# Kernel optimization log

Measured on AMD Instinct MI355X. Metric: run time of the kernel, lower is better.

The kernel has to match this reference:

```python
import jax, jax.numpy as jnp
import numpy as np

S, B, F = 2048, 2, 100          # seq, batch(datasets), n_features
E, NHEAD, NHID, L = 512, 8, 1024, 4  # emsize, heads, ffn hidden, encoder layers
H, NOUT, DEC = 128, 10, 2048    # predicted hidden size, n_out, decoder embed dim
SEP = 1024                      # single_eval_pos
TOTAL = H + F * H + H + H * H + NOUT + H * NOUT  # 30730 flat predicted params


def setup_inputs():
    key = jax.random.key(0)
    ks = jax.random.split(key, 12)
    w = lambda k, sh: jax.random.normal(k, sh, jnp.float32) * 0.02
    z = lambda sh: jnp.zeros(sh, jnp.float32)
    o = lambda sh: jnp.ones(sh, jnp.float32)
    return {
        'x': jax.random.normal(ks[0], (S, B, F), jnp.float32),
        'y': jax.random.normal(ks[1], (S, B), jnp.float32),
        'enc_w': w(ks[2], (E, F)), 'enc_b': z((E,)),
        'yenc_w': w(ks[3], (E, 1)), 'yenc_b': z((E,)),
        'qkv_w': w(ks[4], (L, 3 * E, E)), 'qkv_b': z((L, 3 * E)),
        'out_w': w(ks[5], (L, E, E)), 'out_b': z((L, E)),
        'ln1_g': o((L, E)), 'ln1_b': z((L, E)),
        'ln2_g': o((L, E)), 'ln2_b': z((L, E)),
        'ff1_w': w(ks[6], (L, NHID, E)), 'ff1_b': z((L, NHID)),
        'ff2_w': w(ks[7], (L, E, NHID)), 'ff2_b': z((L, E)),
        'dec_w1': w(ks[8], (DEC, E)), 'dec_b1': z((DEC,)),
        'dec_w2': w(ks[9], (TOTAL, DEC)), 'dec_b2': z((TOTAL,)),
        'single_eval_pos': SEP,
    }


def _ln(x, g, b):
    m = x.mean(-1, keepdims=True)
    v = x.var(-1, keepdims=True)
    return (x - m) / jnp.sqrt(v + 1e-5) * g + b


def _mha(x, wqkv, bqkv, wo, bo):
    s, b, e = x.shape
    hd = e // NHEAD
    qkv = x @ wqkv.T + bqkv                        # [s,b,3e]
    q, k, v = jnp.split(qkv, 3, axis=-1)
    q = q.reshape(s, b, NHEAD, hd)
    k = k.reshape(s, b, NHEAD, hd)
    v = v.reshape(s, b, NHEAD, hd)
    att = jnp.einsum('sbhd,tbhd->bhst', q, k) / np.float32(np.sqrt(hd))
    p = jax.nn.softmax(att, axis=-1)
    o = jnp.einsum('bhst,tbhd->sbhd', p, v).reshape(s, b, e)
    return o @ wo.T + bo


def _forward(x, y, enc_w, enc_b, yenc_w, yenc_b, qkv_w, qkv_b, out_w, out_b,
             ln1_g, ln1_b, ln2_g, ln2_b, ff1_w, ff1_b, ff2_w, ff2_b,
             dec_w1, dec_b1, dec_w2, dec_b2, sep):
    b_sz = x.shape[1]
    # encoders (Linear with replace_nan_by_zero=True)
    x_enc = jnp.nan_to_num(x) @ enc_w.T + enc_b                # [S,B,E]
    y_enc = y[..., None] @ yenc_w.T + yenc_b                   # [S,B,E]
    h = x_enc[:sep] + y_enc[:sep]                              # [sep,B,E]
    # transformer encoder backbone (post-norm, gelu)
    for i in range(L):
        a = _mha(h, qkv_w[i], qkv_b[i], out_w[i], out_b[i])
        h = _ln(h + a, ln1_g[i], ln1_b[i])
        f = jax.nn.gelu(h @ ff1_w[i].T + ff1_b[i]) @ ff2_w[i].T + ff2_b[i]
        h = _ln(h + f, ln2_g[i], ln2_b[i])
    # decoder: mean-pool over train tokens -> MLP -> flat predicted weights
    pooled = h.mean(0)                                         # [B,E]
    d = jax.nn.relu(pooled @ dec_w1.T + dec_b1)
    flat = d @ dec_w2.T + dec_b2                               # [B,TOTAL]
    off = 0
    b1 = flat[:, off:off + H]; off += H
    w1 = flat[:, off:off + F * H].reshape(b_sz, F, H); off += F * H
    b2 = flat[:, off:off + H]; off += H
    w2 = flat[:, off:off + H * H].reshape(b_sz, H, H); off += H * H
    b3 = flat[:, off:off + NOUT]; off += NOUT
    w3 = flat[:, off:off + H * NOUT].reshape(b_sz, H, NOUT)
    # apply predicted per-dataset MLP to test points
    xt = jnp.nan_to_num(x[sep:])                               # [S-sep,B,F]
    t = jnp.einsum('sbf,bfh->sbh', xt, w1) + b1                # (x[...,None]*w1).sum(2)+b1
    t = jnp.einsum('sbh,bhk->sbk', jax.nn.relu(t), w2) + b2
    t = jnp.einsum('sbh,bhk->sbk', jax.nn.relu(t), w3) + b3
    return t                                                   # [S-sep,B,NOUT]


def reference(x, y, enc_w, enc_b, yenc_w, yenc_b, qkv_w, qkv_b, out_w, out_b,
              ln1_g, ln1_b, ln2_g, ln2_b, ff1_w, ff1_b, ff2_w, ff2_b,
              dec_w1, dec_b1, dec_w2, dec_b2, single_eval_pos):
    return _forward(x, y, enc_w, enc_b, yenc_w, yenc_b, qkv_w, qkv_b, out_w, out_b,
                    ln1_g, ln1_b, ln2_g, ln2_b, ff1_w, ff1_b, ff2_w, ff2_b,
                    dec_w1, dec_b1, dec_w2, dec_b2, single_eval_pos)
```

## Files before the change

kernel.cpp:

```cpp
#include <hip/hip_runtime.h>


#define BATCH  2
#define FDIM   100
#define EDIM   512
#define NHEADS 8
#define HD     64
#define NHID   1024
#define NLAYER 4
#define HDIM   128
#define NOUTD  10
#define DECD   2048
#define SEPP   1024
#define TOTALW 30730
#define NTOK   2048

typedef unsigned short u16;
typedef __attribute__((ext_vector_type(8))) short bf16x8;
typedef __attribute__((ext_vector_type(4))) float f32x4;

__device__ __forceinline__ float nanfix(float v) {
    if (isnan(v)) return 0.f;
    if (isinf(v)) return v > 0.f ? 3.4028234663852886e38f : -3.4028234663852886e38f;
    return v;
}
__device__ __forceinline__ u16 f2bf(float f) {
    unsigned u = __float_as_uint(f);
    u += 0x7fffu + ((u >> 16) & 1u);
    return (u16)(u >> 16);
}
__device__ __forceinline__ float bf2f(u16 h) {
    return __uint_as_float(((unsigned)h) << 16);
}
__device__ __forceinline__ bf16x8 scale8(bf16x8 a, float s) {
    bf16x8 r;
    #pragma unroll
    for (int i = 0; i < 8; i++) {
        float v = bf2f((u16)a[i]) * s;
        r[i] = (short)f2bf(v);
    }
    return r;
}

#define GLOAD16(gsrc, ldst) \
    __builtin_amdgcn_global_load_lds( \
        (const __attribute__((address_space(1))) void*)(gsrc), \
        (__attribute__((address_space(3))) void*)(ldst), 16, 0, 0)

__global__ __launch_bounds__(256) void gemm2(
    const u16* __restrict__ A, int lda,
    const u16* __restrict__ B, int ldb,
    void* __restrict__ Cv, int ldc, int cbf,
    int K, long long zCstride, float alpha,
    const float* __restrict__ bias, int act,
    u16* __restrict__ vtout)
{
    __shared__ __align__(16) u16 lds[3][8192];

    int tid = threadIdx.x;
    int lane = tid & 63, w = tid >> 6;
    int wr = w >> 1, wc = w & 1;
    int mBase = blockIdx.y * 64, nBase = blockIdx.x * 64;
    int r16 = lane & 15, kg = lane >> 4;
    long long zk = (long long)blockIdx.z * K;
    long long offC = (long long)blockIdx.z * zCstride;

    int c0 = w * 64 + lane;
    int c1 = 256 + w * 64 + lane;
    int r0 = c0 >> 3, r1 = c1 >> 3;
    int e0 = ((((c0 & 7) * 16) ^ ((r0 & 7) << 4)) >> 1);
    int e1 = ((((c1 & 7) * 16) ^ ((r1 & 7) << 4)) >> 1);
    const u16* sA0 = A + (long long)(mBase + r0) * lda + e0 + zk;
    const u16* sA1 = A + (long long)(mBase + r1) * lda + e1 + zk;
    const u16* sB0 = B + (long long)(nBase + r0) * ldb + e0 + zk;
    const u16* sB1 = B + (long long)(nBase + r1) * ldb + e1 + zk;
    int dA0 = w * 512, dA1 = 2048 + w * 512;
    int dB0 = 4096 + w * 512, dB1 = 6144 + w * 512;

    int ra0 = wr * 32 + r16,      ra1 = wr * 32 + 16 + r16;
    int rb0 = wc * 32 + r16,      rb1 = wc * 32 + 16 + r16;
    int cb0 = kg * 16;
    int cb1 = 64 + kg * 16;
    int oa00 = (ra0 * 128 + (cb0 ^ ((ra0 & 7) << 4))) >> 1;
    int oa01 = (ra0 * 128 + (cb1 ^ ((ra0 & 7) << 4))) >> 1;
    int oa10 = (ra1 * 128 + (cb0 ^ ((ra1 & 7) << 4))) >> 1;
    int oa11 = (ra1 * 128 + (cb1 ^ ((ra1 & 7) << 4))) >> 1;
    int ob00 = 4096 + ((rb0 * 128 + (cb0 ^ ((rb0 & 7) << 4))) >> 1);
    int ob01 = 4096 + ((rb0 * 128 + (cb1 ^ ((rb0 & 7) << 4))) >> 1);
    int ob10 = 4096 + ((rb1 * 128 + (cb0 ^ ((rb1 & 7) << 4))) >> 1);
    int ob11 = 4096 + ((rb1 * 128 + (cb1 ^ ((rb1 & 7) << 4))) >> 1);

    f32x4 acc00 = {0.f, 0.f, 0.f, 0.f};
    f32x4 acc01 = acc00, acc10 = acc00, acc11 = acc00;

    int nt = K >> 6;

#define STAGE2(t, bi) { int ko_ = (t) << 6; \
    GLOAD16(sA0 + ko_, &lds[bi][dA0]); \
    GLOAD16(sA1 + ko_, &lds[bi][dA1]); \
    GLOAD16(sB0 + ko_, &lds[bi][dB0]); \
    GLOAD16(sB1 + ko_, &lds[bi][dB1]); }

    STAGE2(0, 0);
    STAGE2(1, 1);

    int cur = 0;
    for (int t = 0; t < nt; t++) {
        if (t == nt - 1) {
            asm volatile("s_waitcnt vmcnt(0)" ::: "memory");
        } else {
            asm volatile("s_waitcnt vmcnt(4)" ::: "memory");
        }
        __builtin_amdgcn_s_barrier();
        if (t + 2 < nt) {
            int tgt = cur - 1; if (tgt < 0) tgt += 3;
            STAGE2(t + 2, tgt);
        }
        const u16* L = &lds[cur][0];
        bf16x8 a0 = *(const bf16x8*)(L + oa00);
        bf16x8 a1 = *(const bf16x8*)(L + oa10);
        bf16x8 b0 = *(const bf16x8*)(L + ob00);
        bf16x8 b1 = *(const bf16x8*)(L + ob10);
        acc00 = __builtin_amdgcn_mfma_f32_16x16x32_bf16(a0, b0, acc00, 0, 0, 0);
        acc01 = __builtin_amdgcn_mfma_f32_16x16x32_bf16(a0, b1, acc01, 0, 0, 0);
        acc10 = __builtin_amdgcn_mfma_f32_16x16x32_bf16(a1, b0, acc10, 0, 0, 0);
        acc11 = __builtin_amdgcn_mfma_f32_16x16x32_bf16(a1, b1, acc11, 0, 0, 0);
        a0 = *(const bf16x8*)(L + oa01);
        a1 = *(const bf16x8*)(L + oa11);
        b0 = *(const bf16x8*)(L + ob01);
        b1 = *(const bf16x8*)(L + ob11);
        acc00 = __builtin_amdgcn_mfma_f32_16x16x32_bf16(a0, b0, acc00, 0, 0, 0);
        acc01 = __builtin_amdgcn_mfma_f32_16x16x32_bf16(a0, b1, acc01, 0, 0, 0);
        acc10 = __builtin_amdgcn_mfma_f32_16x16x32_bf16(a1, b0, acc10, 0, 0, 0);
        acc11 = __builtin_amdgcn_mfma_f32_16x16x32_bf16(a1, b1, acc11, 0, 0, 0);
        cur++; if (cur == 3) cur = 0;
    }
#undef STAGE2

    if (vtout && nBase >= 1024) {
        u16* T = &lds[0][0];
        __syncthreads();
        #pragma unroll
        for (int i = 0; i < 2; i++) {
            #pragma unroll
            for (int j = 0; j < 2; j++) {
                f32x4 v = (i == 0) ? (j == 0 ? acc00 : acc01) : (j == 0 ? acc10 : acc11);
                int dl = wc * 32 + j * 16 + r16;
                float bv = bias ? bias[nBase + dl] : 0.f;
                #pragma unroll
                for (int r = 0; r < 4; r++) {
                    int ml = wr * 32 + i * 16 + kg * 4 + r;
                    T[ml * 64 + dl] = f2bf(v[r] * alpha + bv);
                }
            }
        }
        __syncthreads();
        int d = tid & 63, cbv = (tid >> 6) & 1, half = tid >> 7;
        int hh = (nBase - 1024) >> 6;
        long long orow = ((long long)(cbv * 8 + hh) * 64 + d) * 1024 + (mBase >> 1) + half * 16;
        bf16x8 v0, v1;
        #pragma unroll
        for (int k = 0; k < 8; k++) {
            v0[k] = (short)T[((half * 16 + k) * 2 + cbv) * 64 + d];
            v1[k] = (short)T[((half * 16 + 8 + k) * 2 + cbv) * 64 + d];
        }
        *(bf16x8*)(vtout + orow) = v0;
        *(bf16x8*)(vtout + orow + 8) = v1;
        return;
    }

    #pragma unroll
    for (int i = 0; i < 2; i++) {
        #pragma unroll
        for (int j = 0; j < 2; j++) {
            f32x4 v = (i == 0) ? (j == 0 ? acc00 : acc01) : (j == 0 ? acc10 : acc11);
            int col = nBase + wc * 32 + j * 16 + r16;
            float bv = bias ? bias[col] : 0.f;
            long long base = offC + (long long)(mBase + wr * 32 + i * 16 + kg * 4) * ldc + col;
            #pragma unroll
            for (int r = 0; r < 4; r++) {
                float c = v[r] * alpha + bv;
                if (act == 2) {
                    float u = 0.7978845608028654f * (c + 0.044715f * c * c * c);
                    c = 0.5f * c * (1.f + tanhf(u));
                }
                if (cbf) ((u16*)Cv)[base + (long long)r * ldc] = f2bf(c);
                else     ((float*)Cv)[base + (long long)r * ldc] = c;
            }
        }
    }
}

__global__ __launch_bounds__(1024) void flash_attn(
    const u16* __restrict__ qkvb, const u16* __restrict__ vtm,
    u16* __restrict__ attnb)
{
    int qt = blockIdx.x;
    int bh = blockIdx.y;
    int cb = bh >> 3, hh = bh & 7;
    int tid = threadIdx.x;
    int w = tid >> 6, lane = tid & 63;
    int p = w & 3, qf = w >> 2;
    int r16 = lane & 15, kg = lane >> 4;

    __shared__ __align__(16) u16 plds[16][2048];
    u16* pl = &plds[w][0];

    int qrow = qt * 64 + p * 16 + r16;
    const u16* qp = qkvb + ((long long)qrow * 2 + cb) * 1536 + hh * 64 + kg * 8;
    bf16x8 qf0 = scale8(*(const bf16x8*)(qp), 0.125f);
    bf16x8 qf1 = scale8(*(const bf16x8*)(qp + 32), 0.125f);

    const u16* kbase = qkvb + (long long)cb * 1536 + 512 + hh * 64;
    const u16* vbase = vtm + ((long long)bh * 64) * 1024;

    f32x4 l = {0.f, 0.f, 0.f, 0.f};
    f32x4 o[4] = {};

    int rb0 = (((r16 * 64 + kg * 8) * 2) ^ ((r16 & 7) << 4)) >> 1;
    int rb1 = (((r16 * 64 + 32 + kg * 8) * 2) ^ ((r16 & 7) << 4)) >> 1;

    for (int kt = qf * 4; kt < qf * 4 + 4; kt++) {
        f32x4 s[4];
        #pragma unroll
        for (int nb = 0; nb < 4; nb++) {
            int key = kt * 64 + nb * 16 + r16;
            const u16* kp = kbase + (long long)key * 3072 + kg * 8;
            bf16x8 kf0 = *(const bf16x8*)(kp);
            bf16x8 kf1 = *(const bf16x8*)(kp + 32);
            f32x4 acc = {};
            acc = __builtin_amdgcn_mfma_f32_16x16x32_bf16(qf0, kf0, acc, 0, 0, 0);
            acc = __builtin_amdgcn_mfma_f32_16x16x32_bf16(qf1, kf1, acc, 0, 0, 0);
            s[nb] = acc;
        }
        f32x4 rs = {};
        #pragma unroll
        for (int nb = 0; nb < 4; nb++)
            #pragma unroll
            for (int r = 0; r < 4; r++) {
                float pv = __expf(s[nb][r]);
                s[nb][r] = pv;
                rs[r] += pv;
            }
        #pragma unroll
        for (int off = 1; off < 16; off <<= 1) {
            #pragma unroll
            for (int r = 0; r < 4; r++) rs[r] += __shfl_xor(rs[r], off);
        }
        #pragma unroll
        for (int r = 0; r < 4; r++) l[r] += rs[r];

        #pragma unroll
        for (int nb = 0; nb < 4; nb++)
            #pragma unroll
            for (int r = 0; r < 4; r++) {
                int row = kg * 4 + r;
                int col = nb * 16 + r16;
                int byi = (((row * 64 + col) * 2) ^ ((row & 7) << 4)) >> 1;
                pl[byi] = f2bf(s[nb][r]);
            }

        bf16x8 pa0 = *(const bf16x8*)(pl + rb0);
        bf16x8 pa1 = *(const bf16x8*)(pl + rb1);
        #pragma unroll
        for (int db = 0; db < 4; db++) {
            const u16* vp = vbase + (long long)(db * 16 + r16) * 1024 + kt * 64 + kg * 8;
            bf16x8 vf0 = *(const bf16x8*)(vp);
            bf16x8 vf1 = *(const bf16x8*)(vp + 32);
            o[db] = __builtin_amdgcn_mfma_f32_16x16x32_bf16(pa0, vf0, o[db], 0, 0, 0);
            o[db] = __builtin_amdgcn_mfma_f32_16x16x32_bf16(pa1, vf1, o[db], 0, 0, 0);
        }
    }

    __syncthreads();
    float* fb = (float*)&plds[0][0];
    if (qf < 3) {
        int base = ((qf * 4 + p) * 64 + lane) * 20;
        #pragma unroll
        for (int r = 0; r < 4; r++) fb[base + r] = l[r];
        #pragma unroll
        for (int db = 0; db < 4; db++)
            #pragma unroll
            for (int r = 0; r < 4; r++) fb[base + 4 + db * 4 + r] = o[db][r];
    }
    __syncthreads();
    if (qf == 3) {
        #pragma unroll
        for (int q2 = 0; q2 < 3; q2++) {
            int base = ((q2 * 4 + p) * 64 + lane) * 20;
            #pragma unroll
            for (int r = 0; r < 4; r++) l[r] += fb[base + r];
            #pragma unroll
            for (int db = 0; db < 4; db++)
                #pragma unroll
                for (int r = 0; r < 4; r++) o[db][r] += fb[base + 4 + db * 4 + r];
        }
        f32x4 linv;
        #pragma unroll
        for (int r = 0; r < 4; r++) linv[r] = 1.f / l[r];
        #pragma unroll
        for (int db = 0; db < 4; db++)
            #pragma unroll
            for (int r = 0; r < 4; r++) {
                float val = o[db][r] * linv[r];
                int row = qt * 64 + p * 16 + kg * 4 + r;
                attnb[((long long)row * 2 + cb) * 512 + hh * 64 + db * 16 + r16] = f2bf(val);
            }
    }
}

__global__ __launch_bounds__(256) void cvt_all(
    const float* __restrict__ s0, const float* __restrict__ s1,
    const float* __restrict__ s2, const float* __restrict__ s3,
    u16* __restrict__ d0, u16* __restrict__ d1,
    u16* __restrict__ d2, u16* __restrict__ d3)
{
    const int n0 = 3145728, n1 = 1048576, n2 = 2097152, n3 = 2097152;
    int i = blockIdx.x * 256 + threadIdx.x;
    int st = gridDim.x * 256;
    for (; i < n0 + n1 + n2 + n3; i += st) {
        if (i < n0) d0[i] = f2bf(s0[i]);
        else if (i < n0 + n1) d1[i - n0] = f2bf(s1[i - n0]);
        else if (i < n0 + n1 + n2) d2[i - n0 - n1] = f2bf(s2[i - n0 - n1]);
        else d3[i - n0 - n1 - n2] = f2bf(s3[i - n0 - n1 - n2]);
    }
}

__global__ __launch_bounds__(512) void encoder_kernel(
    const float* __restrict__ x, const float* __restrict__ y,
    const float* __restrict__ enc_w, const float* __restrict__ enc_b,
    const float* __restrict__ yenc_w, const float* __restrict__ yenc_b,
    float* __restrict__ h, u16* __restrict__ h_bf)
{
    int g = blockIdx.x;
    int tid = threadIdx.x;
    __shared__ float xs[16][FDIM];
    __shared__ float ys[16];
    for (int i = tid; i < 16 * FDIM; i += 512) {
        int tk = i / FDIM, f = i % FDIM;
        xs[tk][f] = nanfix(x[(long long)(g * 16 + tk) * FDIM + f]);
    }
    if (tid < 16) ys[tid] = y[g * 16 + tid];
    __syncthreads();
    float base = enc_b[tid] + yenc_b[tid];
    float yw = yenc_w[tid];
    const float* wr = enc_w + (long long)tid * FDIM;
    float acc[16];
    #pragma unroll
    for (int j = 0; j < 16; j++) acc[j] = 0.f;
    for (int f = 0; f < FDIM; f++) {
        float wv = wr[f];
        #pragma unroll
        for (int j = 0; j < 16; j++) acc[j] = fmaf(xs[j][f], wv, acc[j]);
    }
    #pragma unroll
    for (int j = 0; j < 16; j++) {
        float v = base + ys[j] * yw + acc[j];
        long long t = g * 16 + j;
        h[t * EDIM + tid] = v;
        h_bf[t * EDIM + tid] = f2bf(v);
    }
}

__global__ __launch_bounds__(256) void add_ln3_kernel(
    const float* a, const float* __restrict__ p0, const float* __restrict__ p1,
    const float* __restrict__ cbias,
    const float* __restrict__ g, const float* __restrict__ be,
    float* out, u16* __restrict__ out_bf)
{
    int row = blockIdx.x;
    int tid = threadIdx.x;
    const float* pa = a + (long long)row * EDIM;
    const float* pr0 = p0 + (long long)row * EDIM;
    const float* pr1 = p1 + (long long)row * EDIM;
    float v0 = pa[tid] + pr0[tid] + pr1[tid] + cbias[tid];
    float v1 = pa[tid + 256] + pr0[tid + 256] + pr1[tid + 256] + cbias[tid + 256];
    float s = v0 + v1, q = v0 * v0 + v1 * v1;
    #pragma unroll
    for (int off = 32; off; off >>= 1) {
        s += __shfl_xor(s, off);
        q += __shfl_xor(q, off);
    }
    __shared__ float ss[4], sq[4];
    int w = tid >> 6, lane = tid & 63;
    if (lane == 0) { ss[w] = s; sq[w] = q; }
    __syncthreads();
    s = ss[0] + ss[1] + ss[2] + ss[3];
    q = sq[0] + sq[1] + sq[2] + sq[3];
    float mean = s * (1.f / EDIM);
    float var = q * (1.f / EDIM) - mean * mean;
    float rstd = rsqrtf(var + 1e-5f);
    float o0 = (v0 - mean) * rstd * g[tid] + be[tid];
    float o1 = (v1 - mean) * rstd * g[tid + 256] + be[tid + 256];
    float* po = out + (long long)row * EDIM;
    u16* pb = out_bf + (long long)row * EDIM;
    po[tid] = o0;        po[tid + 256] = o1;
    pb[tid] = f2bf(o0);  pb[tid + 256] = f2bf(o1);
}

__global__ __launch_bounds__(1024) void pool1_kernel(
    const float* __restrict__ h, float* __restrict__ part)
{
    int j = blockIdx.x;
    int idx = threadIdx.x;
    float s = 0.f;
    #pragma unroll 8
    for (int k = 0; k < 32; k++)
        s += h[(long long)(j * 32 + k) * 1024 + idx];
    part[j * 1024 + idx] = s;
}
__global__ __launch_bounds__(1024) void pool2_kernel(
    const float* __restrict__ part, float* __restrict__ pooled)
{
    int idx = threadIdx.x;
    float s = 0.f;
    #pragma unroll 8
    for (int j = 0; j < 32; j++) s += part[j * 1024 + idx];
    pooled[idx] = s * (1.f / 1024.f);
}

__global__ __launch_bounds__(256) void wavedot2_kernel(
    const float* __restrict__ v0, const float* __restrict__ v1,
    const float* __restrict__ W, const float* __restrict__ bias,
    float* __restrict__ out0, float* __restrict__ out1,
    int R, int K, int act)
{
    int gw = (blockIdx.x * 256 + threadIdx.x) >> 6;
    int lane = threadIdx.x & 63;
    int nw = (gridDim.x * 256) >> 6;
    const float4* x0 = (const float4*)v0;
    const float4* x1 = (const float4*)v1;
    for (int r = gw; r < R; r += nw) {
        const float4* w4 = (const float4*)(W + (long long)r * K);
        float a0 = 0.f, a1 = 0.f;
        for (int i = lane; i < (K >> 2); i += 64) {
            float4 w = w4[i];
            float4 p = x0[i];
            float4 q = x1[i];
            a0 += w.x * p.x + w.y * p.y + w.z * p.z + w.w * p.w;
            a1 += w.x * q.x + w.y * q.y + w.z * q.z + w.w * q.w;
        }
        #pragma unroll
        for (int off = 32; off; off >>= 1) {
            a0 += __shfl_xor(a0, off);
            a1 += __shfl_xor(a1, off);
        }
        if (lane == 0) {
            float bb = bias[r];
            float o0 = a0 + bb, o1 = a1 + bb;
            if (act == 1) { o0 = fmaxf(o0, 0.f); o1 = fmaxf(o1, 0.f); }
            out0[r] = o0; out1[r] = o1;
        }
    }
}

__global__ __launch_bounds__(128) void final_mlp_kernel(
    const float* __restrict__ x, const float* __restrict__ flat,
    float* __restrict__ out)
{
    int g = blockIdx.x;
    int b = g >> 7;
    int j0 = (g & 127) * 8;
    int tid = threadIdx.x;
    const float* fl = flat + (long long)b * TOTALW;
    __shared__ float xs[8][FDIM], t1s[8][HDIM], t2s[8][HDIM];
    for (int i = tid; i < 8 * FDIM; i += 128) {
        int j = i / FDIM, f = i % FDIM;
        int t = (j0 + j) * 2 + b;
        xs[j][f] = nanfix(x[(long long)(NTOK + t) * FDIM + f]);
    }
    __syncthreads();
    {
        float acc[8];
        float b1 = fl[tid];
        #pragma unroll
        for (int j = 0; j < 8; j++) acc[j] = b1;
        const float* w1 = fl + HDIM;
        for (int f = 0; f < FDIM; f++) {
            float wv = w1[f * HDIM + tid];
            #pragma unroll
            for (int j = 0; j < 8; j++) acc[j] = fmaf(xs[j][f], wv, acc[j]);
        }
        #pragma unroll
        for (int j = 0; j < 8; j++) t1s[j][tid] = fmaxf(acc[j], 0.f);
    }
    __syncthreads();
    {
        float acc[8];
        float b2 = fl[12928 + tid];
        #pragma unroll
        for (int j = 0; j < 8; j++) acc[j] = b2;
        const float* w2 = fl + 13056;
        for (int hh = 0; hh < HDIM; hh++) {
            float wv = w2[hh * HDIM + tid];
            #pragma unroll
            for (int j = 0; j < 8; j++) acc[j] = fmaf(t1s[j][hh], wv, acc[j]);
        }
        #pragma unroll
        for (int j = 0; j < 8; j++) t2s[j][tid] = fmaxf(acc[j], 0.f);
    }
    __syncthreads();
    if (tid < NOUTD) {
        float acc[8];
        float b3 = fl[29440 + tid];
        #pragma unroll
        for (int j = 0; j < 8; j++) acc[j] = b3;
        const float* w3 = fl + 29450;
        for (int hh = 0; hh < HDIM; hh++) {
            float wv = w3[hh * NOUTD + tid];
            #pragma unroll
            for (int j = 0; j < 8; j++) acc[j] = fmaf(t2s[j][hh], wv, acc[j]);
        }
        #pragma unroll
        for (int j = 0; j < 8; j++) {
            int t = (j0 + j) * 2 + b;
            out[(long long)t * NOUTD + tid] = acc[j];
        }
    }
}

extern "C" void kernel_launch(void* const* d_in, const int* in_sizes, int n_in,
                              void* d_out, int out_size, void* d_ws, size_t ws_size,
                              hipStream_t stream) {
    const float* x      = (const float*)d_in[0];
    const float* y      = (const float*)d_in[1];
    const float* enc_w  = (const float*)d_in[2];
    const float* enc_b  = (const float*)d_in[3];
    const float* yenc_w = (const float*)d_in[4];
    const float* yenc_b = (const float*)d_in[5];
    const float* qkv_w  = (const float*)d_in[6];
    const float* qkv_b  = (const float*)d_in[7];
    const float* out_w  = (const float*)d_in[8];
    const float* out_b  = (const float*)d_in[9];
    const float* ln1_g  = (const float*)d_in[10];
    const float* ln1_b  = (const float*)d_in[11];
    const float* ln2_g  = (const float*)d_in[12];
    const float* ln2_b  = (const float*)d_in[13];
    const float* ff1_w  = (const float*)d_in[14];
    const float* ff1_b  = (const float*)d_in[15];
    const float* ff2_w  = (const float*)d_in[16];
    const float* ff2_b  = (const float*)d_in[17];
    const float* dec_w1 = (const float*)d_in[18];
    const float* dec_b1 = (const float*)d_in[19];
    const float* dec_w2 = (const float*)d_in[20];
    const float* dec_b2 = (const float*)d_in[21];

    float* ws     = (float*)d_ws;
    float* h      = ws;
    u16*   h_bf   = (u16*)(h + 1048576);
    u16*   qkv_bf = h_bf + 1048576;
    u16*   vt     = qkv_bf + 3145728;
    u16*   attn_bf= vt + 1048576;
    u16*   ffb_bf = attn_bf + 1048576;
    u16*   wq     = ffb_bf + 2097152;
    u16*   wo     = wq + 3145728;
    u16*   wf1    = wo + 1048576;
    u16*   wf2    = wf1 + 2097152;
    float* big    = (float*)(wf2 + 2097152);
    float* big2   = big + 1048576;
    float* part   = big2 + 1048576;
    float* pooled = part + 32768;
    float* dbuf   = pooled + 1024;
    float* flat   = dbuf + 4096;

    cvt_all<<<4096, 256, 0, stream>>>(qkv_w, out_w, ff1_w, ff2_w, wq, wo, wf1, wf2);

    encoder_kernel<<<128, 512, 0, stream>>>(x, y, enc_w, enc_b, yenc_w, yenc_b, h, h_bf);

    const long long PSTRIDE = (long long)NTOK * EDIM;

    for (int l = 0; l < NLAYER; l++) {
        gemm2<<<dim3(24, 32, 1), 256, 0, stream>>>(
            h_bf, EDIM, wq + (size_t)l * 786432, EDIM,
            qkv_bf, 1536, 1, EDIM, 0, 1.f, qkv_b + (size_t)l * 1536, 0, vt);

        flash_attn<<<dim3(16, 16), 1024, 0, stream>>>(qkv_bf, vt, attn_bf);

        gemm2<<<dim3(8, 32, 2), 256, 0, stream>>>(
            attn_bf, EDIM, wo + (size_t)l * 262144, EDIM,
            big, EDIM, 0, 256, PSTRIDE, 1.f, nullptr, 0, nullptr);

        add_ln3_kernel<<<NTOK, 256, 0, stream>>>(h, big, big2,
            out_b + (size_t)l * EDIM,
            ln1_g + (size_t)l * EDIM, ln1_b + (size_t)l * EDIM, h, h_bf);

        gemm2<<<dim3(16, 32, 1), 256, 0, stream>>>(
            h_bf, EDIM, wf1 + (size_t)l * 524288, EDIM,
            ffb_bf, NHID, 1, EDIM, 0, 1.f, ff1_b + (size_t)l * NHID, 2, nullptr);

        gemm2<<<dim3(8, 32, 2), 256, 0, stream>>>(
            ffb_bf, NHID, wf2 + (size_t)l * 524288, NHID,
            big, EDIM, 0, 512, PSTRIDE, 1.f, nullptr, 0, nullptr);

        add_ln3_kernel<<<NTOK, 256, 0, stream>>>(h, big, big2,
            ff2_b + (size_t)l * EDIM,
            ln2_g + (size_t)l * EDIM, ln2_b + (size_t)l * EDIM, h, h_bf);
    }

    pool1_kernel<<<32, 1024, 0, stream>>>(h, part);
    pool2_kernel<<<1, 1024, 0, stream>>>(part, pooled);

    wavedot2_kernel<<<512, 256, 0, stream>>>(
        pooled, pooled + EDIM, dec_w1, dec_b1, dbuf, dbuf + DECD, DECD, EDIM, 1);

    wavedot2_kernel<<<7683, 256, 0, stream>>>(
        dbuf, dbuf + DECD, dec_w2, dec_b2, flat, flat + TOTALW, TOTALW, DECD, 0);

    final_mlp_kernel<<<256, 128, 0, stream>>>(x, flat, (float*)d_out);
}
```

Measured before the change: 427.9 us.

## Add 128x128-tile GEMM kernel for QKV and FFN1 projections

Introduces a gemm128 kernel with 128x128 output tiles, double-buffered LDS loads via global_load_lds, and 16 MFMA accumulators per wave. It is used for the QKV and FF1 projections, and the V-transpose epilogue moves from gemm2 into it. Larger tiles raise arithmetic intensity and cut redundant global loads. The cost is fewer blocks (192 and 128 on a large-CU GPU), more register pressure and lower occupancy.

```diff
diff --git a/kernel.cpp b/kernel.cpp
--- a/kernel.cpp
+++ b/kernel.cpp
@@ -47,13 +47,150 @@
         (const __attribute__((address_space(1))) void*)(gsrc), \
         (__attribute__((address_space(3))) void*)(ldst), 16, 0, 0)
 
+__global__ __launch_bounds__(256) void gemm128(
+    const u16* __restrict__ A, int lda,
+    const u16* __restrict__ B, int ldb,
+    u16* __restrict__ C, int ldc,
+    int K, const float* __restrict__ bias, int act,
+    u16* __restrict__ vtout)
+{
+    __shared__ __align__(16) u16 lds[2][16384];
+
+    int tid = threadIdx.x;
+    int lane = tid & 63, w = tid >> 6;
+    int wr = w >> 1, wc = w & 1;
+    int mBase = blockIdx.y * 128, nBase = blockIdx.x * 128;
+    int r16 = lane & 15, kg = lane >> 4;
+
+    const u16* sp[8];
+    #pragma unroll
+    for (int j = 0; j < 8; j++) {
+        int c = j * 256 + tid;
+        int cc = c & 1023;
+        int r = cc >> 3, slot = cc & 7;
+        int elem = (((slot * 16) ^ ((r & 7) << 4)) >> 1);
+        sp[j] = (c < 1024) ? (A + (long long)(mBase + r) * lda + elem)
+                           : (B + (long long)(nBase + r) * ldb + elem);
+    }
+
+    int oa[4][2], ob[4][2];
+    #pragma unroll
+    for (int i = 0; i < 4; i++) {
+        int ra = wr * 64 + i * 16 + r16;
+        int rb = wc * 64 + i * 16 + r16;
+        #pragma unroll
+        for (int k = 0; k < 2; k++) {
+            int cb = k * 64 + kg * 16;
+            oa[i][k] = (ra * 128 + (cb ^ ((ra & 7) << 4))) >> 1;
+            ob[i][k] = 8192 + ((rb * 128 + (cb ^ ((rb & 7) << 4))) >> 1);
+        }
+    }
+
+    f32x4 acc[4][4] = {};
+
+    int nt = K >> 6;
+    #pragma unroll
+    for (int j = 0; j < 8; j++) GLOAD16(sp[j], &lds[0][j * 2048 + w * 512]);
+
+    for (int t = 0; t < nt; t++) {
+        asm volatile("s_waitcnt vmcnt(0)" ::: "memory");
+        __builtin_amdgcn_s_barrier();
+        if (t + 1 < nt) {
+            int ko_ = (t + 1) << 6;
+            #pragma unroll
+            for (int j = 0; j < 8; j++)
+                GLOAD16(sp[j] + ko_, &lds[(t + 1) & 1][j * 2048 + w * 512]);
+        }
+        const u16* L = &lds[t & 1][0];
+        #pragma unroll
+        for (int k = 0; k < 2; k++) {
+            bf16x8 a0 = *(const bf16x8*)(L + oa[0][k]);
+            bf16x8 a1 = *(const bf16x8*)(L + oa[1][k]);
+            bf16x8 a2 = *(const bf16x8*)(L + oa[2][k]);
+            bf16x8 a3 = *(const bf16x8*)(L + oa[3][k]);
+            bf16x8 b0 = *(const bf16x8*)(L + ob[0][k]);
+            bf16x8 b1 = *(const bf16x8*)(L + ob[1][k]);
+            bf16x8 b2 = *(const bf16x8*)(L + ob[2][k]);
+            bf16x8 b3 = *(const bf16x8*)(L + ob[3][k]);
+            acc[0][0] = __builtin_amdgcn_mfma_f32_16x16x32_bf16(a0, b0, acc[0][0], 0, 0, 0);
+            acc[0][1] = __builtin_amdgcn_mfma_f32_16x16x32_bf16(a0, b1, acc[0][1], 0, 0, 0);
+            acc[0][2] = __builtin_amdgcn_mfma_f32_16x16x32_bf16(a0, b2, acc[0][2], 0, 0, 0);
+            acc[0][3] = __builtin_amdgcn_mfma_f32_16x16x32_bf16(a0, b3, acc[0][3], 0, 0, 0);
+            acc[1][0] = __builtin_amdgcn_mfma_f32_16x16x32_bf16(a1, b0, acc[1][0], 0, 0, 0);
+            acc[1][1] = __builtin_amdgcn_mfma_f32_16x16x32_bf16(a1, b1, acc[1][1], 0, 0, 0);
+            acc[1][2] = __builtin_amdgcn_mfma_f32_16x16x32_bf16(a1, b2, acc[1][2], 0, 0, 0);
+            acc[1][3] = __builtin_amdgcn_mfma_f32_16x16x32_bf16(a1, b3, acc[1][3], 0, 0, 0);
+            acc[2][0] = __builtin_amdgcn_mfma_f32_16x16x32_bf16(a2, b0, acc[2][0], 0, 0, 0);
+            acc[2][1] = __builtin_amdgcn_mfma_f32_16x16x32_bf16(a2, b1, acc[2][1], 0, 0, 0);
+            acc[2][2] = __builtin_amdgcn_mfma_f32_16x16x32_bf16(a2, b2, acc[2][2], 0, 0, 0);
+            acc[2][3] = __builtin_amdgcn_mfma_f32_16x16x32_bf16(a2, b3, acc[2][3], 0, 0, 0);
+            acc[3][0] = __builtin_amdgcn_mfma_f32_16x16x32_bf16(a3, b0, acc[3][0], 0, 0, 0);
+            acc[3][1] = __builtin_amdgcn_mfma_f32_16x16x32_bf16(a3, b1, acc[3][1], 0, 0, 0);
+            acc[3][2] = __builtin_amdgcn_mfma_f32_16x16x32_bf16(a3, b2, acc[3][2], 0, 0, 0);
+            acc[3][3] = __builtin_amdgcn_mfma_f32_16x16x32_bf16(a3, b3, acc[3][3], 0, 0, 0);
+        }
+    }
+
+    if (vtout && nBase >= 1024) {
+        u16* T = (u16*)&lds[0][0];
+        __syncthreads();
+        #pragma unroll
+        for (int i = 0; i < 4; i++) {
+            #pragma unroll
+            for (int j = 0; j < 4; j++) {
+                int dl = wc * 64 + j * 16 + r16;
+                float bv = bias ? bias[nBase + dl] : 0.f;
+                #pragma unroll
+                for (int r = 0; r < 4; r++) {
+                    int ml = wr * 64 + i * 16 + kg * 4 + r;
+                    T[dl * 129 + ml] = f2bf(acc[i][j][r] + bv);
+                }
+            }
+        }
+        __syncthreads();
+        int d = tid & 63, hl = (tid >> 6) & 1, cbv = tid >> 7;
+        int hh0 = (nBase - 1024) >> 6;
+        int dl = hl * 64 + d;
+        long long orow = ((long long)(cbv * 8 + hh0 + hl) * 64 + d) * 1024 + (mBase >> 1);
+        #pragma unroll
+        for (int q = 0; q < 8; q++) {
+            bf16x8 v;
+            #pragma unroll
+            for (int e = 0; e < 8; e++) {
+                int k = q * 8 + e;
+                v[e] = (short)T[dl * 129 + k * 2 + cbv];
+            }
+            *(bf16x8*)(vtout + orow + q * 8) = v;
+        }
+        return;
+    }
+
+    #pragma unroll
+    for (int i = 0; i < 4; i++) {
+        #pragma unroll
+        for (int j = 0; j < 4; j++) {
+            int col = nBase + wc * 64 + j * 16 + r16;
+            float bv = bias ? bias[col] : 0.f;
+            long long base = (long long)(mBase + wr * 64 + i * 16 + kg * 4) * ldc + col;
+            #pragma unroll
+            for (int r = 0; r < 4; r++) {
+                float c = acc[i][j][r] + bv;
+                if (act == 2) {
+                    float u = 0.7978845608028654f * (c + 0.044715f * c * c * c);
+                    c = 0.5f * c * (1.f + tanhf(u));
+                }
+                C[base + (long long)r * ldc] = f2bf(c);
+            }
+        }
+    }
+}
+
 __global__ __launch_bounds__(256) void gemm2(
     const u16* __restrict__ A, int lda,
     const u16* __restrict__ B, int ldb,
     void* __restrict__ Cv, int ldc, int cbf,
     int K, long long zCstride, float alpha,
-    const float* __restrict__ bias, int act,
-    u16* __restrict__ vtout)
+    const float* __restrict__ bias, int act)
 {
     __shared__ __align__(16) u16 lds[3][8192];
 
@@ -136,38 +273,6 @@
         cur++; if (cur == 3) cur = 0;
     }
 #undef STAGE2
-
-    if (vtout && nBase >= 1024) {
-        u16* T = &lds[0][0];
-        __syncthreads();
-        #pragma unroll
-        for (int i = 0; i < 2; i++) {
-            #pragma unroll
-            for (int j = 0; j < 2; j++) {
-                f32x4 v = (i == 0) ? (j == 0 ? acc00 : acc01) : (j == 0 ? acc10 : acc11);
-                int dl = wc * 32 + j * 16 + r16;
-                float bv = bias ? bias[nBase + dl] : 0.f;
-                #pragma unroll
-                for (int r = 0; r < 4; r++) {
-                    int ml = wr * 32 + i * 16 + kg * 4 + r;
-                    T[ml * 64 + dl] = f2bf(v[r] * alpha + bv);
-                }
-            }
-        }
-        __syncthreads();
-        int d = tid & 63, cbv = (tid >> 6) & 1, half = tid >> 7;
-        int hh = (nBase - 1024) >> 6;
-        long long orow = ((long long)(cbv * 8 + hh) * 64 + d) * 1024 + (mBase >> 1) + half * 16;
-        bf16x8 v0, v1;
-        #pragma unroll
-        for (int k = 0; k < 8; k++) {
-            v0[k] = (short)T[((half * 16 + k) * 2 + cbv) * 64 + d];
-            v1[k] = (short)T[((half * 16 + 8 + k) * 2 + cbv) * 64 + d];
-        }
-        *(bf16x8*)(vtout + orow) = v0;
-        *(bf16x8*)(vtout + orow + 8) = v1;
-        return;
-    }
 
     #pragma unroll
     for (int i = 0; i < 2; i++) {
@@ -570,27 +675,27 @@
     const long long PSTRIDE = (long long)NTOK * EDIM;
 
     for (int l = 0; l < NLAYER; l++) {
-        gemm2<<<dim3(24, 32, 1), 256, 0, stream>>>(
+        gemm128<<<dim3(12, 16), 256, 0, stream>>>(
             h_bf, EDIM, wq + (size_t)l * 786432, EDIM,
-            qkv_bf, 1536, 1, EDIM, 0, 1.f, qkv_b + (size_t)l * 1536, 0, vt);
+            qkv_bf, 1536, EDIM, qkv_b + (size_t)l * 1536, 0, vt);
 
         flash_attn<<<dim3(16, 16), 1024, 0, stream>>>(qkv_bf, vt, attn_bf);
 
         gemm2<<<dim3(8, 32, 2), 256, 0, stream>>>(
             attn_bf, EDIM, wo + (size_t)l * 262144, EDIM,
-            big, EDIM, 0, 256, PSTRIDE, 1.f, nullptr, 0, nullptr);
+            big, EDIM, 0, 256, PSTRIDE, 1.f, nullptr, 0);
 
         add_ln3_kernel<<<NTOK, 256, 0, stream>>>(h, big, big2,
             out_b + (size_t)l * EDIM,
             ln1_g + (size_t)l * EDIM, ln1_b + (size_t)l * EDIM, h, h_bf);
 
-        gemm2<<<dim3(16, 32, 1), 256, 0, stream>>>(
+        gemm128<<<dim3(8, 16), 256, 0, stream>>>(
             h_bf, EDIM, wf1 + (size_t)l * 524288, EDIM,
-            ffb_bf, NHID, 1, EDIM, 0, 1.f, ff1_b + (size_t)l * NHID, 2, nullptr);
+            ffb_bf, NHID, EDIM, ff1_b + (size_t)l * NHID, 2, nullptr);
 
         gemm2<<<dim3(8, 32, 2), 256, 0, stream>>>(
             ffb_bf, NHID, wf2 + (size_t)l * 524288, NHID,
-            big, EDIM, 0, 512, PSTRIDE, 1.f, nullptr, 0, nullptr);
+            big, EDIM, 0, 512, PSTRIDE, 1.f, nullptr, 0);
 
         add_ln3_kernel<<<NTOK, 256, 0, stream>>>(h, big, big2,
             ff2_b + (size_t)l * EDIM,
```

After: 479.7 us. 1.12x slower.
